# Optimization experiments

Hardware: AMD Instinct MI355X
Metric: run time of the kernel (lower is better)

Reference implementation:

```python
import jax, jax.numpy as jnp
import numpy as np
from jax.ops import segment_sum


def gcn_conv(x, src, dst, W, b, num_nodes):
    # PyG GCNConv: x' = D^{-1/2} (A + I) D^{-1/2} (x @ W) + b
    loops = jnp.arange(num_nodes, dtype=src.dtype)
    s = jnp.concatenate([src, loops])  # source of each edge (incl. self-loops)
    d = jnp.concatenate([dst, loops])  # destination of each edge
    ones = jnp.ones(s.shape[0], dtype=x.dtype)
    deg = segment_sum(ones, d, num_segments=num_nodes)  # in-degree incl. self-loop
    dinv = jnp.where(deg > 0, jax.lax.rsqrt(deg), 0.0)
    norm = dinv[s] * dinv[d]  # [E+N]
    h = x @ W  # [N, C_out] dense transform first (C_out <= C_in typical)
    msg = h[s] * norm[:, None]  # gather + scale  [E+N, C_out]
    out = segment_sum(msg, d, num_segments=num_nodes)  # scatter-add
    return out + b


def setup_inputs() -> dict:
    key = jax.random.key(0)
    k1, k2, k3, k4 = jax.random.split(key, 4)
    N, E = 100000, 1600000
    C_in, C_out = 64, 32
    C_hid = 2 * C_out
    x = jax.random.normal(k1, (N, C_in), dtype=jnp.float32)
    edge_index = jax.random.randint(k2, (2, E), 0, N, dtype=jnp.int64)
    # Glorot-style init for the linear weights, zero bias (PyG defaults)
    W1 = jax.random.normal(k3, (C_in, C_hid), dtype=jnp.float32) * (1.0 / np.sqrt(C_in))
    b1 = jnp.zeros((C_hid,), dtype=jnp.float32)
    W2 = jax.random.normal(k4, (C_hid, C_out), dtype=jnp.float32) * (1.0 / np.sqrt(C_hid))
    b2 = jnp.zeros((C_out,), dtype=jnp.float32)
    return {"x": x, "edge_index": edge_index, "num_nodes": N,
            "W1": W1, "b1": b1, "W2": W2, "b2": b2}


def reference(x, edge_index, num_nodes, W1, b1, W2, b2):
    src, dst = edge_index[0], edge_index[1]
    h = gcn_conv(x, src, dst, W1, b1, num_nodes)
    h = jax.nn.relu(h)
    out = gcn_conv(h, src, dst, W2, b2, num_nodes)
    return out
```

## Files before the change

### kernel.cpp

```cpp
#include <hip/hip_runtime.h>


constexpr int CAP = 2048;
constexpr int NBMAX = 2048;
constexpr int SBCAP = 40960;
constexpr int NSBMAX = 64;
constexpr float QS = 2048.f;
constexpr float QSI = 1.f / 2048.f;

__device__ inline int sxlo(unsigned u) { return (int)(short)(u & 0xffffu); }
__device__ inline int sxhi(unsigned u) { return ((int)u) >> 16; }

__global__ __launch_bounds__(256) void p1a(const int* __restrict__ src,
                                           const int* __restrict__ dst,
                                           int* __restrict__ sbCursor,
                                           unsigned* __restrict__ stg1, int E, int NSB) {
    __shared__ int cnt[NSBMAX];
    __shared__ int cur[NSBMAX];
    int tid = threadIdx.x;
    if (tid < NSBMAX) cnt[tid] = 0;
    __syncthreads();
    int e0 = blockIdx.x * 2048;
    unsigned dv[8];
#pragma unroll
    for (int k = 0; k < 8; ++k) {
        int e = e0 + k * 256 + tid;
        dv[k] = 0u;
        if (e < E) {
            dv[k] = (unsigned)dst[e];
            atomicAdd(&cnt[dv[k] >> 11], 1);
        }
    }
    __syncthreads();
    if (tid < NSB) {
        int c = cnt[tid];
        cur[tid] = c ? atomicAdd(&sbCursor[tid], c) : 0;
    }
    __syncthreads();
#pragma unroll
    for (int k = 0; k < 8; ++k) {
        int e = e0 + k * 256 + tid;
        if (e < E) {
            unsigned d = dv[k];
            int b = d >> 11;
            int slot = atomicAdd(&cur[b], 1);
            if (slot < SBCAP)
                stg1[(size_t)b * SBCAP + slot] = ((unsigned)src[e] << 11) | (d & 2047u);
        }
    }
}

__global__ __launch_bounds__(256) void p1b(const unsigned* __restrict__ stg1,
                                           const int* __restrict__ sbCursor,
                                           int* __restrict__ bucketCursor,
                                           unsigned* __restrict__ staging) {
    __shared__ int cnt[32];
    __shared__ int cur[32];
    int b = blockIdx.x >> 4;
    int s = blockIdx.x & 15;
    int tid = threadIdx.x;
    if (tid < 32) cnt[tid] = 0;
    __syncthreads();
    int sz = sbCursor[b];
    if (sz > SBCAP) sz = SBCAP;
    int lo = (sz * s) >> 4, hi = (sz * (s + 1)) >> 4;
    const unsigned* st = stg1 + (size_t)b * SBCAP;
    for (int i = lo + tid; i < hi; i += 256) atomicAdd(&cnt[(st[i] >> 6) & 31u], 1);
    __syncthreads();
    if (tid < 32) {
        int c = cnt[tid];
        cur[tid] = c ? atomicAdd(&bucketCursor[b * 32 + tid], c) : 0;
    }
    __syncthreads();
    for (int i = lo + tid; i < hi; i += 256) {
        unsigned w = st[i];
        int f = (w >> 6) & 31u;
        int slot = atomicAdd(&cur[f], 1);
        if (slot < CAP)
            staging[(size_t)(b * 32 + f) * CAP + slot] = ((w >> 11) << 6) | (w & 63u);
    }
}

__global__ __launch_bounds__(256) void gemm1(const float* __restrict__ X,
                                             const float* __restrict__ W,
                                             const unsigned* __restrict__ staging,
                                             const int* __restrict__ bucketCursor,
                                             float* __restrict__ dinv,
                                             unsigned short* __restrict__ Hout, int N) {
    constexpr int XS = 65;
    __shared__ float Xs[128 * XS];
    __shared__ float Ws[64 * 64];
    __shared__ int degs[128];
    int tid = threadIdx.x;
    int b = blockIdx.x;
    int rowBase = b * 128;
    if (tid < 128) degs[tid] = 0;
    __syncthreads();
    {
        int sz0 = bucketCursor[2 * b];
        if (sz0 > CAP) sz0 = CAP;
        const unsigned* st0 = staging + (size_t)(2 * b) * CAP;
        for (int i = tid; i < sz0; i += 256) atomicAdd(&degs[st0[i] & 63u], 1);
        int sz1 = bucketCursor[2 * b + 1];
        if (sz1 > CAP) sz1 = CAP;
        const unsigned* st1 = staging + (size_t)(2 * b + 1) * CAP;
        for (int i = tid; i < sz1; i += 256) atomicAdd(&degs[64 + (st1[i] & 63u)], 1);
    }
    const float4* Wv = (const float4*)W;
    float4* Wsv = (float4*)Ws;
    for (int i = tid; i < 64 * 64 / 4; i += 256) Wsv[i] = Wv[i];
    const float4* Xv = (const float4*)X;
    for (int v = tid; v < 128 * 16; v += 256) {
        int r = v >> 4, j = v & 15;
        int gr = rowBase + r;
        float4 t = make_float4(0.f, 0.f, 0.f, 0.f);
        if (gr < N) t = Xv[(size_t)gr * 16 + j];
        int bb = r * XS + j * 4;
        Xs[bb] = t.x;
        Xs[bb + 1] = t.y;
        Xs[bb + 2] = t.z;
        Xs[bb + 3] = t.w;
    }
    __syncthreads();
    if (tid < 128) {
        int gn = rowBase + tid;
        if (gn < N) dinv[gn] = rsqrtf((float)(degs[tid] + 1));
    }
    int cg = tid % 8, rg = tid / 8;
    int c0 = cg * 8, r0 = rg * 4;
    float acc[4][8];
#pragma unroll
    for (int i = 0; i < 4; ++i)
#pragma unroll
        for (int j = 0; j < 8; ++j) acc[i][j] = 0.f;
#pragma unroll 8
    for (int k = 0; k < 64; ++k) {
        float4 w0 = *(const float4*)&Ws[k * 64 + c0];
        float4 w1 = *(const float4*)&Ws[k * 64 + c0 + 4];
        float xr[4];
#pragma unroll
        for (int i = 0; i < 4; ++i) xr[i] = Xs[(r0 + i) * XS + k];
#pragma unroll
        for (int i = 0; i < 4; ++i) {
            acc[i][0] = fmaf(xr[i], w0.x, acc[i][0]);
            acc[i][1] = fmaf(xr[i], w0.y, acc[i][1]);
            acc[i][2] = fmaf(xr[i], w0.z, acc[i][2]);
            acc[i][3] = fmaf(xr[i], w0.w, acc[i][3]);
            acc[i][4] = fmaf(xr[i], w1.x, acc[i][4]);
            acc[i][5] = fmaf(xr[i], w1.y, acc[i][5]);
            acc[i][6] = fmaf(xr[i], w1.z, acc[i][6]);
            acc[i][7] = fmaf(xr[i], w1.w, acc[i][7]);
        }
    }
#pragma unroll
    for (int i = 0; i < 4; ++i) {
        int row = rowBase + r0 + i;
        if (row >= N) continue;
        float dq = rsqrtf((float)(degs[r0 + i] + 1)) * QS;
        unsigned short* rp = Hout + (size_t)row * 64 + cg;
#pragma unroll
        for (int j = 0; j < 8; ++j) {
            rp[8 * j] = (unsigned short)(short)(int)(acc[i][j] * dq);
        }
    }
}

__global__ __launch_bounds__(256) void agg1_gemm2(
    const uint4* __restrict__ hs1, const unsigned* __restrict__ staging,
    const int* __restrict__ bucketCursor, const float* __restrict__ dinv,
    const float* __restrict__ b1, const float* __restrict__ W2,
    unsigned short* __restrict__ h2, int N) {
    constexpr int S1 = 65;
    __shared__ int acc[64 * S1];
    __shared__ float Ws[64 * 32];
    __shared__ float b1s[64];
    __shared__ float dns[64];
    int b = blockIdx.x, tid = threadIdx.x;
    int gbase = b * 64;
    const float4* Wv = (const float4*)W2;
    float4* Wsv = (float4*)Ws;
    for (int i = tid; i < 64 * 32 / 4; i += 256) Wsv[i] = Wv[i];
    if (tid < 64) b1s[tid] = QS * b1[tid];
    if (tid >= 64 && tid < 128) {
        int gn = gbase + tid - 64;
        dns[tid - 64] = (gn < N) ? dinv[gn] : 0.f;
    }
    for (int v = tid; v < 64 * 8; v += 256) {
        int n = v >> 3, j = v & 7;
        int s0 = 0, s1 = 0, s2 = 0, s3 = 0, s4 = 0, s5 = 0, s6 = 0, s7 = 0;
        if (gbase + n < N) {
            uint4 u = hs1[(size_t)(gbase + n) * 8 + j];
            s0 = sxlo(u.x); s1 = sxhi(u.x);
            s2 = sxlo(u.y); s3 = sxhi(u.y);
            s4 = sxlo(u.z); s5 = sxhi(u.z);
            s6 = sxlo(u.w); s7 = sxhi(u.w);
        }
        int* dp = &acc[n * S1 + j];
        dp[0] = s0;  dp[8] = s1;  dp[16] = s2; dp[24] = s3;
        dp[32] = s4; dp[40] = s5; dp[48] = s6; dp[56] = s7;
    }
    __syncthreads();
    int size = bucketCursor[b];
    if (size > CAP) size = CAP;
    const unsigned* st = staging + (size_t)b * CAP;
    int g = tid >> 3, q = tid & 7;
#define ADD8(NN, U)                          \
    {                                        \
        int* ap = &acc[(int)(NN) * S1 + q];  \
        atomicAdd(ap + 0,  sxlo((U).x));     \
        atomicAdd(ap + 8,  sxhi((U).x));     \
        atomicAdd(ap + 16, sxlo((U).y));     \
        atomicAdd(ap + 24, sxhi((U).y));     \
        atomicAdd(ap + 32, sxlo((U).z));     \
        atomicAdd(ap + 40, sxhi((U).z));     \
        atomicAdd(ap + 48, sxlo((U).w));     \
        atomicAdd(ap + 56, sxhi((U).w));     \
    }
    int i = g;
    for (; i + 480 < size; i += 512) {
        unsigned w[16];
        uint4 u[16];
#pragma unroll
        for (int k = 0; k < 16; ++k) w[k] = st[i + 32 * k];
#pragma unroll
        for (int k = 0; k < 16; ++k) u[k] = hs1[(size_t)(w[k] >> 6) * 8 + q];
#pragma unroll
        for (int k = 0; k < 16; ++k) ADD8(w[k] & 63u, u[k])
    }
    for (; i + 224 < size; i += 256) {
        unsigned w[8];
        uint4 u[8];
#pragma unroll
        for (int k = 0; k < 8; ++k) w[k] = st[i + 32 * k];
#pragma unroll
        for (int k = 0; k < 8; ++k) u[k] = hs1[(size_t)(w[k] >> 6) * 8 + q];
#pragma unroll
        for (int k = 0; k < 8; ++k) ADD8(w[k] & 63u, u[k])
    }
    for (; i < size; i += 32) {
        unsigned w = st[i];
        uint4 u = hs1[(size_t)(w >> 6) * 8 + q];
        ADD8(w & 63u, u)
    }
#undef ADD8
    __syncthreads();
    float* af = (float*)acc;
    for (int v = tid; v < 64 * 64; v += 256) {
        int n = v >> 6, c = v & 63;
        af[n * S1 + c] = fmaxf(fmaf((float)acc[n * S1 + c], dns[n], b1s[c]), 0.f);
    }
    __syncthreads();
    int cg = tid & 3, rg = tid >> 2;
    int c0 = cg * 8;
    float a2[8];
#pragma unroll
    for (int j = 0; j < 8; ++j) a2[j] = 0.f;
#pragma unroll 8
    for (int k = 0; k < 64; ++k) {
        float4 w0 = *(const float4*)&Ws[k * 32 + c0];
        float4 w1 = *(const float4*)&Ws[k * 32 + c0 + 4];
        float x0 = af[rg * S1 + k];
        a2[0] = fmaf(x0, w0.x, a2[0]);
        a2[1] = fmaf(x0, w0.y, a2[1]);
        a2[2] = fmaf(x0, w0.z, a2[2]);
        a2[3] = fmaf(x0, w0.w, a2[3]);
        a2[4] = fmaf(x0, w1.x, a2[4]);
        a2[5] = fmaf(x0, w1.y, a2[5]);
        a2[6] = fmaf(x0, w1.z, a2[6]);
        a2[7] = fmaf(x0, w1.w, a2[7]);
    }
    int row = gbase + rg;
    if (row < N) {
        float dn = dns[rg];
        unsigned short* rp = h2 + (size_t)row * 32;
#pragma unroll
        for (int j = 0; j < 8; ++j) {
            rp[8 * (j & 3) + 2 * cg + (j >> 2)] = (unsigned short)(short)(int)(a2[j] * dn);
        }
    }
}

__global__ __launch_bounds__(256) void agg2(const uint4* __restrict__ hs2,
                                            const unsigned* __restrict__ staging,
                                            const int* __restrict__ bucketCursor,
                                            const float* __restrict__ dinv,
                                            const float* __restrict__ b2,
                                            float* __restrict__ out, int N) {
    constexpr int S2 = 33;
    __shared__ int acc[64 * S2];
    __shared__ float b2s[32];
    int b = blockIdx.x, tid = threadIdx.x;
    int gbase = b * 64;
    if (tid < 32) b2s[tid] = b2[tid];
    for (int v = tid; v < 64 * 4; v += 256) {
        int n = v >> 2, j = v & 3;
        int s0 = 0, s1 = 0, s2 = 0, s3 = 0, s4 = 0, s5 = 0, s6 = 0, s7 = 0;
        if (gbase + n < N) {
            uint4 u = hs2[(size_t)(gbase + n) * 4 + j];
            s0 = sxlo(u.x); s1 = sxhi(u.x);
            s2 = sxlo(u.y); s3 = sxhi(u.y);
            s4 = sxlo(u.z); s5 = sxhi(u.z);
            s6 = sxlo(u.w); s7 = sxhi(u.w);
        }
        int* dp = &acc[n * S2 + j];
        dp[0] = s0;  dp[4] = s1;  dp[8] = s2;  dp[12] = s3;
        dp[16] = s4; dp[20] = s5; dp[24] = s6; dp[28] = s7;
    }
    __syncthreads();
    int size = bucketCursor[b];
    if (size > CAP) size = CAP;
    const unsigned* st = staging + (size_t)b * CAP;
    int g = tid >> 2, q = tid & 3;
#define ADD8(NN, U)                          \
    {                                        \
        int* ap = &acc[(int)(NN) * S2 + q];  \
        atomicAdd(ap + 0,  sxlo((U).x));     \
        atomicAdd(ap + 4,  sxhi((U).x));     \
        atomicAdd(ap + 8,  sxlo((U).y));     \
        atomicAdd(ap + 12, sxhi((U).y));     \
        atomicAdd(ap + 16, sxlo((U).z));     \
        atomicAdd(ap + 20, sxhi((U).z));     \
        atomicAdd(ap + 24, sxlo((U).w));     \
        atomicAdd(ap + 28, sxhi((U).w));     \
    }
    int i = g;
    for (; i + 448 < size; i += 512) {
        unsigned w[8];
        uint4 u[8];
#pragma unroll
        for (int k = 0; k < 8; ++k) w[k] = st[i + 64 * k];
#pragma unroll
        for (int k = 0; k < 8; ++k) u[k] = hs2[(size_t)(w[k] >> 6) * 4 + q];
#pragma unroll
        for (int k = 0; k < 8; ++k) ADD8(w[k] & 63u, u[k])
    }
    for (; i < size; i += 64) {
        unsigned w = st[i];
        uint4 u = hs2[(size_t)(w >> 6) * 4 + q];
        ADD8(w & 63u, u)
    }
#undef ADD8
    __syncthreads();
    for (int v = tid; v < 64 * 32; v += 256) {
        int n = v >> 5, c = v & 31;
        int gn = gbase + n;
        if (gn >= N) continue;
        out[(size_t)gn * 32 + c] = fmaf((float)acc[n * S2 + c], dinv[gn] * QSI, b2s[c]);
    }
}

extern "C" void kernel_launch(void* const* d_in, const int* in_sizes, int n_in,
                              void* d_out, int out_size, void* d_ws, size_t ws_size,
                              hipStream_t stream) {
    const float* x = (const float*)d_in[0];
    const int* ei = (const int*)d_in[1];
    const float* W1 = (const float*)d_in[3];
    const float* b1 = (const float*)d_in[4];
    const float* W2 = (const float*)d_in[5];
    const float* b2 = (const float*)d_in[6];

    constexpr int CIN = 64, CHID = 64, COUT = 32;
    const int N = in_sizes[0] / CIN;
    const int E = in_sizes[1] / 2;
    const int* src = ei;
    const int* dst = ei + E;
    const int NSB = (N + 2047) >> 11;
    const int NBT = NSB * 32;

    char* p = (char*)d_ws;
    auto carve = [&](size_t bytes) -> void* {
        void* q = (void*)p;
        p += (bytes + 255) & ~(size_t)255;
        return q;
    };
    int* sbCursor = (int*)carve((size_t)NSBMAX * 4);
    int* bucketCursor = (int*)carve((size_t)NBMAX * 4);
    float* dinv = (float*)carve((size_t)N * 4);
    unsigned* stg1 = (unsigned*)carve((size_t)NSB * SBCAP * 4);
    unsigned* staging = (unsigned*)carve((size_t)NBT * CAP * 4);
    unsigned* h1 = (unsigned*)carve((size_t)N * CHID * 2);
    unsigned* h2 = stg1;

    size_t zbytes = (size_t)((char*)(bucketCursor + NBMAX) - (char*)sbCursor);
    hipMemsetAsync(sbCursor, 0, zbytes, stream);
    p1a<<<(E + 2047) / 2048, 256, 0, stream>>>(src, dst, sbCursor, stg1, E, NSB);
    p1b<<<NSB * 16, 256, 0, stream>>>(stg1, sbCursor, bucketCursor, staging);
    gemm1<<<(N + 127) / 128, 256, 0, stream>>>(x, W1, staging, bucketCursor, dinv,
                                               (unsigned short*)h1, N);
    agg1_gemm2<<<NBT, 256, 0, stream>>>((const uint4*)h1, staging, bucketCursor, dinv,
                                        b1, W2, (unsigned short*)h2, N);
    agg2<<<NBT, 256, 0, stream>>>((const uint4*)h2, staging, bucketCursor, dinv, b2,
                                  (float*)d_out, N);
}
```

Measured before the change: 209.2 us.

## Split layer-2 features into two channel halves and double agg2 blocks

The second-layer features are now stored as two separate 16-channel int16 planes instead of one interleaved 32-channel array. agg2 launches twice as many blocks, and each block aggregates one channel half over the same destination bucket. Each per-node gather is 32 bytes instead of 64, and the halved per-block shared accumulator should improve occupancy and parallelism. In exchange, the edge staging list is read twice and the gathers are narrower, which adds more random-access transactions.

```diff
diff --git a/kernel.cpp b/kernel.cpp
--- a/kernel.cpp
+++ b/kernel.cpp
@@ -169,7 +169,7 @@
     const uint4* __restrict__ hs1, const unsigned* __restrict__ staging,
     const int* __restrict__ bucketCursor, const float* __restrict__ dinv,
     const float* __restrict__ b1, const float* __restrict__ W2,
-    unsigned short* __restrict__ h2, int N) {
+    unsigned short* __restrict__ h2a, unsigned short* __restrict__ h2b, int N) {
     constexpr int S1 = 65;
     __shared__ int acc[64 * S1];
     __shared__ float Ws[64 * 32];
@@ -272,80 +272,86 @@
     int row = gbase + rg;
     if (row < N) {
         float dn = dns[rg];
-        unsigned short* rp = h2 + (size_t)row * 32;
+        unsigned short* rp = ((cg >> 1) ? h2b : h2a) + (size_t)row * 16;
+        int boff = 4 * (cg & 1);
 #pragma unroll
         for (int j = 0; j < 8; ++j) {
-            rp[8 * (j & 3) + 2 * cg + (j >> 2)] = (unsigned short)(short)(int)(a2[j] * dn);
-        }
-    }
-}
-
-__global__ __launch_bounds__(256) void agg2(const uint4* __restrict__ hs2,
+            rp[8 * (j & 1) + boff + (j >> 1)] = (unsigned short)(short)(int)(a2[j] * dn);
+        }
+    }
+}
+
+__global__ __launch_bounds__(256) void agg2(const uint4* __restrict__ h2a,
+                                            const uint4* __restrict__ h2b,
                                             const unsigned* __restrict__ staging,
                                             const int* __restrict__ bucketCursor,
                                             const float* __restrict__ dinv,
                                             const float* __restrict__ b2,
                                             float* __restrict__ out, int N) {
-    constexpr int S2 = 33;
+    constexpr int S2 = 17;
     __shared__ int acc[64 * S2];
-    __shared__ float b2s[32];
-    int b = blockIdx.x, tid = threadIdx.x;
+    __shared__ float b2s[16];
+    int x = blockIdx.x, tid = threadIdx.x;
+    int half = (x >> 2) & 1;
+    int b = (x >> 3) * 4 + (x & 3);
+    const uint4* hs = half ? h2b : h2a;
     int gbase = b * 64;
-    if (tid < 32) b2s[tid] = b2[tid];
-    for (int v = tid; v < 64 * 4; v += 256) {
-        int n = v >> 2, j = v & 3;
+    if (tid < 16) b2s[tid] = b2[half * 16 + tid];
+    for (int v = tid; v < 64 * 2; v += 256) {
+        int n = v >> 1, j = v & 1;
         int s0 = 0, s1 = 0, s2 = 0, s3 = 0, s4 = 0, s5 = 0, s6 = 0, s7 = 0;
         if (gbase + n < N) {
-            uint4 u = hs2[(size_t)(gbase + n) * 4 + j];
+            uint4 u = hs[(size_t)(gbase + n) * 2 + j];
             s0 = sxlo(u.x); s1 = sxhi(u.x);
             s2 = sxlo(u.y); s3 = sxhi(u.y);
             s4 = sxlo(u.z); s5 = sxhi(u.z);
             s6 = sxlo(u.w); s7 = sxhi(u.w);
         }
         int* dp = &acc[n * S2 + j];
-        dp[0] = s0;  dp[4] = s1;  dp[8] = s2;  dp[12] = s3;
-        dp[16] = s4; dp[20] = s5; dp[24] = s6; dp[28] = s7;
+        dp[0] = s0;  dp[2] = s1;  dp[4] = s2;  dp[6] = s3;
+        dp[8] = s4;  dp[10] = s5; dp[12] = s6; dp[14] = s7;
     }
     __syncthreads();
     int size = bucketCursor[b];
     if (size > CAP) size = CAP;
     const unsigned* st = staging + (size_t)b * CAP;
-    int g = tid >> 2, q = tid & 3;
+    int g = tid >> 1, q = tid & 1;
 #define ADD8(NN, U)                          \
     {                                        \
         int* ap = &acc[(int)(NN) * S2 + q];  \
         atomicAdd(ap + 0,  sxlo((U).x));     \
-        atomicAdd(ap + 4,  sxhi((U).x));     \
-        atomicAdd(ap + 8,  sxlo((U).y));     \
-        atomicAdd(ap + 12, sxhi((U).y));     \
-        atomicAdd(ap + 16, sxlo((U).z));     \
-        atomicAdd(ap + 20, sxhi((U).z));     \
-        atomicAdd(ap + 24, sxlo((U).w));     \
-        atomicAdd(ap + 28, sxhi((U).w));     \
+        atomicAdd(ap + 2,  sxhi((U).x));     \
+        atomicAdd(ap + 4,  sxlo((U).y));     \
+        atomicAdd(ap + 6,  sxhi((U).y));     \
+        atomicAdd(ap + 8,  sxlo((U).z));     \
+        atomicAdd(ap + 10, sxhi((U).z));     \
+        atomicAdd(ap + 12, sxlo((U).w));     \
+        atomicAdd(ap + 14, sxhi((U).w));     \
     }
     int i = g;
-    for (; i + 448 < size; i += 512) {
+    for (; i + 896 < size; i += 1024) {
         unsigned w[8];
         uint4 u[8];
 #pragma unroll
-        for (int k = 0; k < 8; ++k) w[k] = st[i + 64 * k];
-#pragma unroll
-        for (int k = 0; k < 8; ++k) u[k] = hs2[(size_t)(w[k] >> 6) * 4 + q];
+        for (int k = 0; k < 8; ++k) w[k] = st[i + 128 * k];
+#pragma unroll
+        for (int k = 0; k < 8; ++k) u[k] = hs[(size_t)(w[k] >> 6) * 2 + q];
 #pragma unroll
         for (int k = 0; k < 8; ++k) ADD8(w[k] & 63u, u[k])
     }
-    for (; i < size; i += 64) {
+    for (; i < size; i += 128) {
         unsigned w = st[i];
-        uint4 u = hs2[(size_t)(w >> 6) * 4 + q];
+        uint4 u = hs[(size_t)(w >> 6) * 2 + q];
         ADD8(w & 63u, u)
     }
 #undef ADD8
     __syncthreads();
-    for (int v = tid; v < 64 * 32; v += 256) {
-        int n = v >> 5, c = v & 31;
+    for (int v = tid; v < 64 * 16; v += 256) {
+        int n = v >> 4, c = v & 15;
         int gn = gbase + n;
         if (gn >= N) continue;
-        out[(size_t)gn * 32 + c] = fmaf((float)acc[n * S2 + c], dinv[gn] * QSI, b2s[c]);
+        out[(size_t)gn * 32 + half * 16 + c] =
+            fmaf((float)acc[n * S2 + c], dinv[gn] * QSI, b2s[c]);
     }
 }
 
@@ -379,7 +385,8 @@
     unsigned* stg1 = (unsigned*)carve((size_t)NSB * SBCAP * 4);
     unsigned* staging = (unsigned*)carve((size_t)NBT * CAP * 4);
     unsigned* h1 = (unsigned*)carve((size_t)N * CHID * 2);
-    unsigned* h2 = stg1;
+    unsigned short* h2a = (unsigned short*)stg1;
+    unsigned short* h2b = h2a + (size_t)N * 16;
 
     size_t zbytes = (size_t)((char*)(bucketCursor + NBMAX) - (char*)sbCursor);
     hipMemsetAsync(sbCursor, 0, zbytes, stream);
@@ -388,7 +395,7 @@
     gemm1<<<(N + 127) / 128, 256, 0, stream>>>(x, W1, staging, bucketCursor, dinv,
                                                (unsigned short*)h1, N);
     agg1_gemm2<<<NBT, 256, 0, stream>>>((const uint4*)h1, staging, bucketCursor, dinv,
-                                        b1, W2, (unsigned short*)h2, N);
-    agg2<<<NBT, 256, 0, stream>>>((const uint4*)h2, staging, bucketCursor, dinv, b2,
-                                  (float*)d_out, N);
-}
+                                        b1, W2, h2a, h2b, N);
+    agg2<<<NBT * 2, 256, 0, stream>>>((const uint4*)h2a, (const uint4*)h2b, staging,
+                                      bucketCursor, dinv, b2, (float*)d_out, N);
+}
```

Measured after the change: 213.3 us. No clear change (+2.0%).
